# Performance work log

Measured on AMD Instinct MI355X. Metric: run time of the kernel, lower is better.

## Reference

```python
import jax, jax.numpy as jnp
import numpy as np

B, S, D, V, ML = 8, 1024, 768, 32000, 2000
EPS = 1e-5


def layernorm(x, g, b):
    mu = jnp.mean(x, axis=-1, keepdims=True)
    var = jnp.mean(jnp.square(x - mu), axis=-1, keepdims=True)
    return (x - mu) * jax.lax.rsqrt(var + EPS) * g + b


def setup_inputs() -> dict:
    key = jax.random.key(0)
    ks = jax.random.split(key, 16)
    idx = jax.random.randint(ks[0], (B, S), 0, V)
    attention_mask = jax.random.randint(ks[1], (B, S), 0, 2).astype(jnp.int32)
    # guarantee at least one valid key per row so softmax rows are finite
    attention_mask = attention_mask.at[:, 0].set(1)
    s = 0.02
    return {
        "idx": idx,
        "attention_mask": attention_mask,
        "emb": jax.random.normal(ks[2], (V, D), jnp.float32) * s,
        "pos_emb": jax.random.normal(ks[3], (ML, D), jnp.float32) * s,
        "Wq": jax.random.normal(ks[4], (D, D), jnp.float32) * s,
        "Wk": jax.random.normal(ks[5], (D, D), jnp.float32) * s,
        "Wv": jax.random.normal(ks[6], (D, D), jnp.float32) * s,
        "ln1_g": jnp.ones((D,), jnp.float32),
        "ln1_b": jnp.zeros((D,), jnp.float32),
        "W1": jax.random.normal(ks[7], (D, D), jnp.float32) * s,
        "b1": jnp.zeros((D,), jnp.float32),
        "W2": jax.random.normal(ks[8], (D, D), jnp.float32) * s,
        "b2": jnp.zeros((D,), jnp.float32),
        "ln2_g": jnp.ones((D,), jnp.float32),
        "ln2_b": jnp.zeros((D,), jnp.float32),
    }


def reference(idx, attention_mask, emb, pos_emb, Wq, Wk, Wv, ln1_g, ln1_b,
              W1, b1, W2, b2, ln2_g, ln2_b):
    seq_len = idx.shape[1]
    x = emb[idx] + pos_emb[:seq_len]                       # [B,S,D]
    q = x @ Wq                                             # [B,S,D]
    k = x @ Wk
    v = x @ Wv
    att = jnp.einsum('bqd,bkd->bqk', q, k) * (D ** -0.5)   # [B,S,S]
    att = jnp.where(attention_mask[:, None, :] == 0, -jnp.inf, att)
    a = jax.nn.softmax(att, axis=-1) @ v                   # [B,S,D]
    x = layernorm(a, ln1_g, ln1_b)
    h = jax.nn.gelu(x @ W1 + b1, approximate=False)        # exact GELU (torch default)
    h = jax.nn.gelu(h @ W2 + b2, approximate=False)
    return layernorm(h, ln2_g, ln2_b)
```

## Files before the change

kernel.cpp:

```cpp
#include <hip/hip_runtime.h>
#include <hip/hip_bf16.h>
#include <math.h>

typedef __bf16 bf16;
typedef __attribute__((ext_vector_type(8))) __bf16 bf16x8;
typedef __attribute__((ext_vector_type(4))) __bf16 bf16x4;
typedef __attribute__((ext_vector_type(4))) float f32x4;

#define NB 8
#define SEQ 1024
#define DIM 768
#define ROWS (NB*SEQ)

__device__ __forceinline__ float gelu_exact(float x){
  return 0.5f * x * (1.0f + erff(x * 0.70710678118654752440f));
}

__device__ __forceinline__ void gload_lds16(const void* g, void* l){
  __builtin_amdgcn_global_load_lds((const __attribute__((address_space(1))) void*)g,
                                   (__attribute__((address_space(3))) void*)l, 16, 0, 0);
}

__global__ __launch_bounds__(192)
void k_embed(const int* __restrict__ idx, const float* __restrict__ emb,
             const float* __restrict__ pos, bf16* __restrict__ xo){
  const int row = blockIdx.x;
  const int s = row & (SEQ-1);
  const int tok = idx[row];
  const float* e = emb + (long)tok*DIM;
  const float* p = pos + (long)s*DIM;
  bf16* o = xo + (long)row*DIM;
  const int tid = threadIdx.x;
  f32x4 ev = *(const f32x4*)(e + tid*4);
  f32x4 pv = *(const f32x4*)(p + tid*4);
  bf16x4 ov;
  ov[0]=(bf16)(ev[0]+pv[0]); ov[1]=(bf16)(ev[1]+pv[1]);
  ov[2]=(bf16)(ev[2]+pv[2]); ov[3]=(bf16)(ev[3]+pv[3]);
  *(bf16x4*)(o + tid*4) = ov;
}

__global__ __launch_bounds__(256)
void k_transpose_w(const float* __restrict__ Wq, const float* __restrict__ Wk,
                   const float* __restrict__ Wv, const float* __restrict__ W1,
                   const float* __restrict__ W2,
                   bf16* __restrict__ Wqkvt, bf16* __restrict__ W1t, bf16* __restrict__ W2t){
  __shared__ float t[32][33];
  const int z = blockIdx.z;
  const float* src = (z==0)?Wq:(z==1)?Wk:(z==2)?Wv:(z==3)?W1:W2;
  bf16* dst = (z<3) ? (Wqkvt + (size_t)z*768*768) : ((z==3)?W1t:W2t);
  const int n0 = blockIdx.x*32, k0 = blockIdx.y*32;
  const int tx = threadIdx.x, ty = threadIdx.y;
  #pragma unroll
  for (int i=0;i<4;i++)
    t[ty+i*8][tx] = src[(long)(k0+ty+i*8)*768 + n0 + tx];
  __syncthreads();
  #pragma unroll
  for (int i=0;i<4;i++)
    dst[(long)(n0+ty+i*8)*768 + k0 + tx] = (bf16)t[tx][ty+i*8];
}

__global__ __launch_bounds__(256)
void k_transpose_v(const bf16* __restrict__ qkv, bf16* __restrict__ vT){
  __shared__ bf16 t[32][33];
  const int b = blockIdx.z;
  const int s0 = blockIdx.x*32, d0 = blockIdx.y*32;
  const int tx = threadIdx.x, ty = threadIdx.y;
  const bf16* src = qkv + (long)b*SEQ*2304 + 1536;
  bf16* dst = vT + (long)b*DIM*SEQ;
  #pragma unroll
  for (int i=0;i<4;i++)
    t[ty+i*8][tx] = src[(long)(s0+ty+i*8)*2304 + d0 + tx];
  __syncthreads();
  #pragma unroll
  for (int i=0;i<4;i++)
    dst[(long)(d0+ty+i*8)*SEQ + s0 + tx] = t[tx][ty+i*8];
}

template<int EPI>
__global__ __launch_bounds__(256, 2)
void k_gemm2p(const bf16* __restrict__ A, int lda, long sA,
              const bf16* __restrict__ Bt, int ldb, long sB,
              void* __restrict__ Cv, int ldc, long sC,
              int K,
              const float* __restrict__ bias,
              const int* __restrict__ mask, int maskStride,
              const float* __restrict__ rowinv,
              float scale)
{
  __shared__ __align__(16) bf16 As[2][128][32];
  __shared__ __align__(16) bf16 Bs[2][128][32];

  const int bz = blockIdx.z;
  A  += (long)bz * sA;
  Bt += (long)bz * sB;
  const int m0 = blockIdx.x * 128;
  const int n0 = blockIdx.y * 128;

  const int tid  = threadIdx.x;
  const int lane = tid & 63;
  const int w    = tid >> 6;

  const int st_row = w*16 + (lane>>2);
  const int st_col = (lane&3)*8;
  const bf16* Ag0 = A  + (long)(m0 + st_row)*lda + st_col;
  const bf16* Bg0 = Bt + (long)(n0 + st_row)*ldb + st_col;

  const int nk = K >> 5;

  f32x4 acc[4][4];
  const f32x4 zero = {0.f,0.f,0.f,0.f};
  #pragma unroll
  for (int i=0;i<4;i++)
    #pragma unroll
    for (int j=0;j<4;j++) acc[i][j] = zero;

  const int wr = (w>>1)*64;
  const int wc = (w&1)*64;
  const int fr = lane & 15;
  const int fk = (lane>>4)*8;

  {
    char* lA = (char*)&As[0][0][0] + w*1024;
    char* lB = (char*)&Bs[0][0][0] + w*1024;
    gload_lds16(Ag0,                lA);
    gload_lds16(Ag0 + (long)64*lda, lA + 4096);
    gload_lds16(Bg0,                lB);
    gload_lds16(Bg0 + (long)64*ldb, lB + 4096);
  }

  int buf = 0;
  for (int kt=0; kt<nk; kt++){
    __syncthreads();
    if (kt+1 < nk){
      const bf16* Ag = Ag0 + (kt+1)*32;
      const bf16* Bg = Bg0 + (kt+1)*32;
      char* lA = (char*)&As[buf^1][0][0] + w*1024;
      char* lB = (char*)&Bs[buf^1][0][0] + w*1024;
      gload_lds16(Ag,                lA);
      gload_lds16(Ag + (long)64*lda, lA + 4096);
      gload_lds16(Bg,                lB);
      gload_lds16(Bg + (long)64*ldb, lB + 4096);
    }
    bf16x8 af[4], bfv[4];
    #pragma unroll
    for (int t=0;t<4;t++){
      af[t]  = *(const bf16x8*)&As[buf][wr + t*16 + fr][fk];
      bfv[t] = *(const bf16x8*)&Bs[buf][wc + t*16 + fr][fk];
    }
    #pragma unroll
    for (int mt=0;mt<4;mt++)
      #pragma unroll
      for (int nt=0;nt<4;nt++)
        acc[mt][nt] = __builtin_amdgcn_mfma_f32_16x16x32_bf16(af[mt], bfv[nt], acc[mt][nt], 0, 0, 0);
    buf ^= 1;
  }

  const int cm0 = m0 + wr + ((lane>>4)<<2);
  const int cn0 = n0 + wc + fr;
  const long cb = (long)bz * sC;
  const int* mk = (EPI==3) ? (mask + (long)bz*maskStride) : nullptr;
  const float* rinv = (EPI==4) ? (rowinv + (long)bz*SEQ) : nullptr;

  #pragma unroll
  for (int mt=0;mt<4;mt++){
    #pragma unroll
    for (int nt=0;nt<4;nt++){
      #pragma unroll
      for (int r=0;r<4;r++){
        const int m = cm0 + mt*16 + r;
        const int n = cn0 + nt*16;
        const long o = cb + (long)m*ldc + n;
        float c = acc[mt][nt][r];
        if (EPI == 0){
          ((bf16*)Cv)[o] = (bf16)c;
        } else if (EPI == 1){
          ((bf16*)Cv)[o] = (bf16)gelu_exact(c + bias[n]);
        } else if (EPI == 2){
          ((float*)Cv)[o] = gelu_exact(c + bias[n]);
        } else if (EPI == 3){
          ((bf16*)Cv)[o] = (bf16)((mk[n] != 0) ? expf(c*scale) : 0.0f);
        } else {
          ((float*)Cv)[o] = c * rinv[m];
        }
      }
    }
  }
}

__global__ __launch_bounds__(256)
void k_rowsum(const bf16* __restrict__ P, float* __restrict__ rowinv){
  __shared__ float red[4];
  const int row = blockIdx.x;
  const bf16* p = P + (long)row * SEQ;
  const int tid = threadIdx.x;
  bf16x4 v4 = *(const bf16x4*)(p + tid*4);
  float s = (float)v4[0] + (float)v4[1] + (float)v4[2] + (float)v4[3];
  #pragma unroll
  for (int o=32;o>0;o>>=1) s += __shfl_xor(s, o);
  if ((tid&63)==0) red[tid>>6] = s;
  __syncthreads();
  if (tid==0){
    rowinv[row] = 1.0f / (red[0]+red[1]+red[2]+red[3]);
  }
}

template<int OUT_BF16>
__global__ __launch_bounds__(256)
void k_layernorm(const float* __restrict__ X, const float* __restrict__ g,
                 const float* __restrict__ b, void* __restrict__ Yv){
  __shared__ float red[4];
  __shared__ float red2[4];
  const int row = blockIdx.x;
  const float* x = X + (long)row*DIM;
  const int tid = threadIdx.x;
  float v0=x[tid], v1=x[tid+256], v2=x[tid+512];
  float s = v0+v1+v2;
  #pragma unroll
  for (int o=32;o>0;o>>=1) s += __shfl_xor(s, o);
  if ((tid&63)==0) red[tid>>6] = s;
  __syncthreads();
  s = red[0]+red[1]+red[2]+red[3];
  const float mu = s * (1.0f/768.0f);
  const float d0=v0-mu, d1=v1-mu, d2=v2-mu;
  float q = d0*d0+d1*d1+d2*d2;
  #pragma unroll
  for (int o=32;o>0;o>>=1) q += __shfl_xor(q, o);
  if ((tid&63)==0) red2[tid>>6] = q;
  __syncthreads();
  q = red2[0]+red2[1]+red2[2]+red2[3];
  const float r = rsqrtf(q*(1.0f/768.0f) + 1e-5f);
  const float y0 = d0*r*g[tid]     + b[tid];
  const float y1 = d1*r*g[tid+256] + b[tid+256];
  const float y2 = d2*r*g[tid+512] + b[tid+512];
  if (OUT_BF16){
    bf16* Y = (bf16*)Yv;
    Y[(long)row*DIM+tid]=(bf16)y0; Y[(long)row*DIM+tid+256]=(bf16)y1; Y[(long)row*DIM+tid+512]=(bf16)y2;
  } else {
    float* Y = (float*)Yv;
    Y[(long)row*DIM+tid]=y0; Y[(long)row*DIM+tid+256]=y1; Y[(long)row*DIM+tid+512]=y2;
  }
}

extern "C" void kernel_launch(void* const* d_in, const int* in_sizes, int n_in,
                              void* d_out, int out_size, void* d_ws, size_t ws_size,
                              hipStream_t stream)
{
  (void)in_sizes; (void)n_in; (void)out_size; (void)ws_size;
  const int*   idx  = (const int*)d_in[0];
  const int*   am   = (const int*)d_in[1];
  const float* emb  = (const float*)d_in[2];
  const float* pos  = (const float*)d_in[3];
  const float* Wq   = (const float*)d_in[4];
  const float* Wk   = (const float*)d_in[5];
  const float* Wv   = (const float*)d_in[6];
  const float* ln1g = (const float*)d_in[7];
  const float* ln1b = (const float*)d_in[8];
  const float* W1   = (const float*)d_in[9];
  const float* b1   = (const float*)d_in[10];
  const float* W2   = (const float*)d_in[11];
  const float* b2   = (const float*)d_in[12];
  const float* ln2g = (const float*)d_in[13];
  const float* ln2b = (const float*)d_in[14];

  char* ws = (char*)d_ws;
  size_t off = 0;
  auto take = [&](size_t bytes)->char*{
    char* p = ws + off;
    off += (bytes + 255) & ~(size_t)255;
    return p;
  };
  bf16*  Wqkvt = (bf16*) take((size_t)2304*768*2);
  bf16*  W1t   = (bf16*) take((size_t)768*768*2);
  bf16*  W2t   = (bf16*) take((size_t)768*768*2);
  bf16*  xbf   = (bf16*) take((size_t)ROWS*DIM*2);
  bf16*  qkv   = (bf16*) take((size_t)ROWS*2304*2);
  bf16*  vT    = (bf16*) take((size_t)NB*DIM*SEQ*2);
  bf16*  P     = (bf16*) take((size_t)NB*SEQ*SEQ*2);
  float* rowiv = (float*)take((size_t)ROWS*4);
  float* aout  = (float*)take((size_t)ROWS*DIM*4);
  bf16*  x1    = (bf16*) take((size_t)ROWS*DIM*2);
  bf16*  h1    = (bf16*) take((size_t)ROWS*DIM*2);
  float* h2    = (float*)take((size_t)ROWS*DIM*4);
  float* out   = (float*)d_out;

  k_transpose_w<<<dim3(24,24,5), dim3(32,8), 0, stream>>>(Wq,Wk,Wv,W1,W2, Wqkvt,W1t,W2t);

  k_embed<<<ROWS, 192, 0, stream>>>(idx, emb, pos, xbf);

  k_gemm2p<0><<<dim3(64,18,1), 256, 0, stream>>>(xbf,768,0L, Wqkvt,768,0L,
                                                 qkv,2304,0L, 768,
                                                 nullptr, nullptr,0, nullptr, 1.0f);

  k_transpose_v<<<dim3(32,24,8), dim3(32,8), 0, stream>>>(qkv, vT);

  k_gemm2p<3><<<dim3(8,8,8), 256, 0, stream>>>(
      qkv,     2304, (long)SEQ*2304,
      qkv+768, 2304, (long)SEQ*2304,
      P,       SEQ,  (long)SEQ*SEQ,
      768, nullptr, am, SEQ, nullptr, 0.03608439182435161f);

  k_rowsum<<<ROWS, 256, 0, stream>>>(P, rowiv);

  k_gemm2p<4><<<dim3(8,6,8), 256, 0, stream>>>(
      P,    SEQ, (long)SEQ*SEQ,
      vT,   SEQ, (long)DIM*SEQ,
      aout, DIM, (long)SEQ*DIM,
      1024, nullptr, nullptr,0, rowiv, 1.0f);

  k_layernorm<1><<<ROWS, 256, 0, stream>>>(aout, ln1g, ln1b, x1);

  k_gemm2p<1><<<dim3(64,6,1), 256, 0, stream>>>(x1,768,0L, W1t,768,0L, h1,768,0L,
                                                768, b1, nullptr,0, nullptr, 1.0f);
  k_gemm2p<2><<<dim3(64,6,1), 256, 0, stream>>>(h1,768,0L, W2t,768,0L, h2,768,0L,
                                                768, b2, nullptr,0, nullptr, 1.0f);

  k_layernorm<0><<<ROWS, 256, 0, stream>>>(h2, ln2g, ln2b, out);
}
```

Before: 352.3 us.

## Fuse softmax rowsum into score GEMM, use bf16 intermediates, remap workgroups across XCDs

The score GEMM epilogue now reduces each row's exp values across lanes and atomically adds them into a zeroed rowsum buffer, which removes the separate rowsum kernel. The attention output and second MLP activation are stored as bf16 instead of fp32, halving their memory traffic, and layernorm gains a bf16-input variant. GEMM workgroup indices are remapped in chunks of eight, apparently so neighbouring tiles land on the same XCD to improve L2 locality. The costs are atomic contention, an extra memset, and reduced precision in the intermediates feeding layernorm.

```diff
diff --git a/kernel.cpp b/kernel.cpp
--- a/kernel.cpp
+++ b/kernel.cpp
@@ -84,7 +84,7 @@
               int K,
               const float* __restrict__ bias,
               const int* __restrict__ mask, int maskStride,
-              const float* __restrict__ rowinv,
+              float* __restrict__ rowsum,
               float scale)
 {
   __shared__ __align__(16) bf16 As[2][128][32];
@@ -93,8 +93,14 @@
   const int bz = blockIdx.z;
   A  += (long)bz * sA;
   Bt += (long)bz * sB;
-  const int m0 = blockIdx.x * 128;
-  const int n0 = blockIdx.y * 128;
+
+  const int gx = gridDim.x;
+  const int nwg = gx * gridDim.y;
+  const int chunk = nwg >> 3;
+  const int flat = blockIdx.y*gx + blockIdx.x;
+  const int logical = (flat & 7)*chunk + (flat >> 3);
+  const int m0 = (logical % gx) * 128;
+  const int n0 = (logical / gx) * 128;
 
   const int tid  = threadIdx.x;
   const int lane = tid & 63;
@@ -158,15 +164,54 @@
   const int cm0 = m0 + wr + ((lane>>4)<<2);
   const int cn0 = n0 + wc + fr;
   const long cb = (long)bz * sC;
-  const int* mk = (EPI==3) ? (mask + (long)bz*maskStride) : nullptr;
-  const float* rinv = (EPI==4) ? (rowinv + (long)bz*SEQ) : nullptr;
+
+  if (EPI == 3){
+    const int* mk = mask + (long)bz*maskStride;
+    float rowpart[4][4];
+    #pragma unroll
+    for (int mt=0;mt<4;mt++)
+      #pragma unroll
+      for (int r=0;r<4;r++) rowpart[mt][r] = 0.f;
+    #pragma unroll
+    for (int mt=0;mt<4;mt++){
+      #pragma unroll
+      for (int nt=0;nt<4;nt++){
+        #pragma unroll
+        for (int r=0;r<4;r++){
+          const int m = cm0 + mt*16 + r;
+          const int n = cn0 + nt*16;
+          float p = (mk[n] != 0) ? expf(acc[mt][nt][r]*scale) : 0.0f;
+          bf16 pb = (bf16)p;
+          ((bf16*)Cv)[cb + (long)m*ldc + n] = pb;
+          rowpart[mt][r] += (float)pb;
+        }
+      }
+    }
+    #pragma unroll
+    for (int mt=0;mt<4;mt++){
+      #pragma unroll
+      for (int r=0;r<4;r++){
+        float v = rowpart[mt][r];
+        v += __shfl_xor(v, 1);
+        v += __shfl_xor(v, 2);
+        v += __shfl_xor(v, 4);
+        v += __shfl_xor(v, 8);
+        if ((lane & 15) == 0)
+          atomicAdd(&rowsum[(long)bz*SEQ + cm0 + mt*16 + r], v);
+      }
+    }
+    return;
+  }
 
   #pragma unroll
   for (int mt=0;mt<4;mt++){
     #pragma unroll
-    for (int nt=0;nt<4;nt++){
-      #pragma unroll
-      for (int r=0;r<4;r++){
+    for (int r=0;r<4;r++){
+      float rinv = 1.0f;
+      if (EPI == 4)
+        rinv = 1.0f / rowsum[(long)bz*SEQ + cm0 + mt*16 + r];
+      #pragma unroll
+      for (int nt=0;nt<4;nt++){
         const int m = cm0 + mt*16 + r;
         const int n = cn0 + nt*16;
         const long o = cb + (long)m*ldc + n;
@@ -175,45 +220,30 @@
           ((bf16*)Cv)[o] = (bf16)c;
         } else if (EPI == 1){
           ((bf16*)Cv)[o] = (bf16)gelu_exact(c + bias[n]);
-        } else if (EPI == 2){
-          ((float*)Cv)[o] = gelu_exact(c + bias[n]);
-        } else if (EPI == 3){
-          ((bf16*)Cv)[o] = (bf16)((mk[n] != 0) ? expf(c*scale) : 0.0f);
         } else {
-          ((float*)Cv)[o] = c * rinv[m];
+          ((bf16*)Cv)[o] = (bf16)(c * rinv);
         }
       }
     }
   }
 }
 
+template<int IN_BF16, int OUT_BF16>
 __global__ __launch_bounds__(256)
-void k_rowsum(const bf16* __restrict__ P, float* __restrict__ rowinv){
-  __shared__ float red[4];
-  const int row = blockIdx.x;
-  const bf16* p = P + (long)row * SEQ;
-  const int tid = threadIdx.x;
-  bf16x4 v4 = *(const bf16x4*)(p + tid*4);
-  float s = (float)v4[0] + (float)v4[1] + (float)v4[2] + (float)v4[3];
-  #pragma unroll
-  for (int o=32;o>0;o>>=1) s += __shfl_xor(s, o);
-  if ((tid&63)==0) red[tid>>6] = s;
-  __syncthreads();
-  if (tid==0){
-    rowinv[row] = 1.0f / (red[0]+red[1]+red[2]+red[3]);
-  }
-}
-
-template<int OUT_BF16>
-__global__ __launch_bounds__(256)
-void k_layernorm(const float* __restrict__ X, const float* __restrict__ g,
+void k_layernorm(const void* __restrict__ Xv, const float* __restrict__ g,
                  const float* __restrict__ b, void* __restrict__ Yv){
   __shared__ float red[4];
   __shared__ float red2[4];
   const int row = blockIdx.x;
-  const float* x = X + (long)row*DIM;
   const int tid = threadIdx.x;
-  float v0=x[tid], v1=x[tid+256], v2=x[tid+512];
+  float v0, v1, v2;
+  if (IN_BF16){
+    const bf16* x = (const bf16*)Xv + (long)row*DIM;
+    v0=(float)x[tid]; v1=(float)x[tid+256]; v2=(float)x[tid+512];
+  } else {
+    const float* x = (const float*)Xv + (long)row*DIM;
+    v0=x[tid]; v1=x[tid+256]; v2=x[tid+512];
+  }
   float s = v0+v1+v2;
   #pragma unroll
   for (int o=32;o>0;o>>=1) s += __shfl_xor(s, o);
@@ -276,12 +306,14 @@
   bf16*  qkv   = (bf16*) take((size_t)ROWS*2304*2);
   bf16*  vT    = (bf16*) take((size_t)NB*DIM*SEQ*2);
   bf16*  P     = (bf16*) take((size_t)NB*SEQ*SEQ*2);
-  float* rowiv = (float*)take((size_t)ROWS*4);
-  float* aout  = (float*)take((size_t)ROWS*DIM*4);
+  float* rsum  = (float*)take((size_t)ROWS*4);
+  bf16*  aout  = (bf16*) take((size_t)ROWS*DIM*2);
   bf16*  x1    = (bf16*) take((size_t)ROWS*DIM*2);
   bf16*  h1    = (bf16*) take((size_t)ROWS*DIM*2);
-  float* h2    = (float*)take((size_t)ROWS*DIM*4);
+  bf16*  h2    = (bf16*) take((size_t)ROWS*DIM*2);
   float* out   = (float*)d_out;
+
+  hipMemsetAsync(rsum, 0, (size_t)ROWS*4, stream);
 
   k_transpose_w<<<dim3(24,24,5), dim3(32,8), 0, stream>>>(Wq,Wk,Wv,W1,W2, Wqkvt,W1t,W2t);
 
@@ -297,22 +329,20 @@
       qkv,     2304, (long)SEQ*2304,
       qkv+768, 2304, (long)SEQ*2304,
       P,       SEQ,  (long)SEQ*SEQ,
-      768, nullptr, am, SEQ, nullptr, 0.03608439182435161f);
-
-  k_rowsum<<<ROWS, 256, 0, stream>>>(P, rowiv);
+      768, nullptr, am, SEQ, rsum, 0.03608439182435161f);
 
   k_gemm2p<4><<<dim3(8,6,8), 256, 0, stream>>>(
       P,    SEQ, (long)SEQ*SEQ,
       vT,   SEQ, (long)DIM*SEQ,
       aout, DIM, (long)SEQ*DIM,
-      1024, nullptr, nullptr,0, rowiv, 1.0f);
-
-  k_layernorm<1><<<ROWS, 256, 0, stream>>>(aout, ln1g, ln1b, x1);
+      1024, nullptr, nullptr,0, rsum, 1.0f);
+
+  k_layernorm<1,1><<<ROWS, 256, 0, stream>>>(aout, ln1g, ln1b, x1);
 
   k_gemm2p<1><<<dim3(64,6,1), 256, 0, stream>>>(x1,768,0L, W1t,768,0L, h1,768,0L,
                                                 768, b1, nullptr,0, nullptr, 1.0f);
-  k_gemm2p<2><<<dim3(64,6,1), 256, 0, stream>>>(h1,768,0L, W2t,768,0L, h2,768,0L,
+  k_gemm2p<1><<<dim3(64,6,1), 256, 0, stream>>>(h1,768,0L, W2t,768,0L, h2,768,0L,
                                                 768, b2, nullptr,0, nullptr, 1.0f);
 
-  k_layernorm<0><<<ROWS, 256, 0, stream>>>(h2, ln2g, ln2b, out);
-}
+  k_layernorm<1,0><<<ROWS, 256, 0, stream>>>(h2, ln2g, ln2b, out);
+}
```

Measured after the change: 356.3 us. About the same (+1.1%).
